# Performance work log

Hardware: AMD Instinct MI355X
Metric: run time of the kernel (lower is better)

## Reference

```python
import jax, jax.numpy as jnp
import numpy as np

N_BASIS = 128
N_CHANNELS = 256
DECAY_INIT = 3.0
B, T, V = 4, 4096, 1024


def setup_inputs() -> dict:
    key = jax.random.key(0)
    ks = jax.random.split(key, 6)
    std = 0.02
    return {
        "x": jax.random.normal(ks[0], (B, T, V), dtype=jnp.float32),
        "basis": jax.random.normal(ks[1], (V, 2 * N_BASIS), dtype=jnp.float32),
        "q_coeffs": jax.random.normal(ks[2], (N_CHANNELS, 2 * N_BASIS), dtype=jnp.float32) * std,
        "k_coeffs": jax.random.normal(ks[3], (N_CHANNELS, 2 * N_BASIS), dtype=jnp.float32) * std,
        "v_coeffs": jax.random.normal(ks[4], (N_CHANNELS, 2 * N_BASIS), dtype=jnp.float32) * std,
        "o_coeffs": jax.random.normal(ks[5], (N_CHANNELS, 2 * N_BASIS), dtype=jnp.float32) * std,
        "decay_logit": jnp.asarray(DECAY_INIT, dtype=jnp.float32),
        "out_scale": jnp.asarray(0.1, dtype=jnp.float32),
    }


def reference(x, basis, q_coeffs, k_coeffs, v_coeffs, o_coeffs, decay_logit, out_scale):
    dtype = x.dtype
    # FourierProjection: basis [V, 2*nb] @ coeffs.T [2*nb, C] -> [V, C]
    q_w = (basis @ q_coeffs.T).astype(dtype)
    k_w = (basis @ k_coeffs.T).astype(dtype)
    v_w = (basis @ v_coeffs.T).astype(dtype)
    o_w = (basis @ o_coeffs.T).astype(dtype)

    queries = jnp.einsum('btv,vc->btc', x, q_w)   # [B,T,C]
    keys    = jnp.einsum('btv,vc->btc', x, k_w)
    values  = jnp.einsum('btv,vc->btc', x, v_w)

    scores = jnp.einsum('btc,bsc->bts', queries, keys)  # [B,T,T]

    decay = jax.nn.sigmoid(decay_logit)
    t = x.shape[1]
    pos = jnp.arange(t)
    diff = pos[None, :] - pos[:, None]           # diff[i,j] = j - i
    causal_mask = (diff > 0)
    exponent = jnp.maximum(diff.astype(jnp.float32) - 1.0, 0.0)
    decay_weights = (decay ** exponent) * causal_mask.astype(jnp.float32)

    scores = scores * decay_weights.astype(dtype)[None]
    retrieved = jnp.einsum('bts,bsc->btc', scores, values)  # [B,T,C]
    out = jnp.einsum('btc,vc->btv', retrieved, o_w) * out_scale.astype(dtype)
    return out
```

## Files before the change

### kernel.cpp

```cpp
#include <hip/hip_runtime.h>
#include <math.h>
#include <stdint.h>

#define B_ 4
#define T_ 4096
#define V_ 1024
#define C_ 256
#define WINDOW 512

typedef __bf16 bf16x8 __attribute__((ext_vector_type(8)));
typedef float f32x4 __attribute__((ext_vector_type(4)));
typedef unsigned short us8 __attribute__((ext_vector_type(8)));

__device__ __forceinline__ void gld16(const void* g, void* l) {
  auto gp = reinterpret_cast<const __attribute__((address_space(1))) uint32_t*>(
      reinterpret_cast<uintptr_t>(g));
  auto lp = reinterpret_cast<__attribute__((address_space(3))) uint32_t*>(
      reinterpret_cast<uintptr_t>(l));
  __builtin_amdgcn_global_load_lds(gp, lp, 16, 0, 0);
}

__device__ __forceinline__ unsigned short f2bf(float f) {
  union { float f; unsigned u; } v; v.f = f;
  unsigned r = v.u + 0x7fffu + ((v.u >> 16) & 1u);
  return (unsigned short)(r >> 16);
}

__global__ __launch_bounds__(256) void prep_all(
    const float* __restrict__ qc, const float* __restrict__ kc,
    const float* __restrict__ vc, const float* __restrict__ basis,
    const float* __restrict__ oc, unsigned short* __restrict__ W3,
    unsigned short* __restrict__ bsT, unsigned short* __restrict__ owb) {
  const int tid = threadIdx.x;
  const int z = blockIdx.y;
  if (z == 0) {
    const size_t i = ((size_t)blockIdx.x * 256 + tid) * 8;
    const float* src = (i < 65536) ? qc + i
                     : (i < 131072) ? kc + (i - 65536) : vc + (i - 131072);
    const float4 a = *(const float4*)src;
    const float4 b = *(const float4*)(src + 4);
    us8 o;
    o[0] = f2bf(a.x); o[1] = f2bf(a.y); o[2] = f2bf(a.z); o[3] = f2bf(a.w);
    o[4] = f2bf(b.x); o[5] = f2bf(b.y); o[6] = f2bf(b.z); o[7] = f2bf(b.w);
    *(us8*)(W3 + i) = o;
  } else if (z == 1) {
    if (blockIdx.x >= 64) return;
    __shared__ unsigned short tile[64][65];
    const int rb = blockIdx.x >> 2, cb = blockIdx.x & 3;
#pragma unroll
    for (int r2 = 0; r2 < 2; ++r2) {
      const int idx = r2 * 256 + tid;
      const int row = idx >> 3, p = idx & 7;
      const float4 a = *(const float4*)(basis + (size_t)(rb * 64 + row) * 256 +
                                        cb * 64 + p * 8);
      const float4 b = *(const float4*)(basis + (size_t)(rb * 64 + row) * 256 +
                                        cb * 64 + p * 8 + 4);
      tile[row][p * 8 + 0] = f2bf(a.x); tile[row][p * 8 + 1] = f2bf(a.y);
      tile[row][p * 8 + 2] = f2bf(a.z); tile[row][p * 8 + 3] = f2bf(a.w);
      tile[row][p * 8 + 4] = f2bf(b.x); tile[row][p * 8 + 5] = f2bf(b.y);
      tile[row][p * 8 + 6] = f2bf(b.z); tile[row][p * 8 + 7] = f2bf(b.w);
    }
    __syncthreads();
#pragma unroll
    for (int r2 = 0; r2 < 2; ++r2) {
      const int idx = r2 * 256 + tid;
      const int c = idx >> 3, p = idx & 7;
      us8 v;
#pragma unroll
      for (int j = 0; j < 8; ++j) v[j] = tile[p * 8 + j][c];
      *(us8*)(bsT + ((size_t)(cb * 64 + c)) * 1024 + rb * 64 + p * 8) = v;
    }
  } else {
    if (blockIdx.x >= 64) return;
    __shared__ float As[16][65];
    __shared__ float Bs[16][65];
    const int bm = blockIdx.x >> 2, bn = blockIdx.x & 3;
    const int m0 = bm * 64, n0 = bn * 64;
    const int tm = tid >> 4, tn = tid & 15;
    float acc[4][4] = {};
    for (int k0 = 0; k0 < 256; k0 += 16) {
#pragma unroll
      for (int r = 0; r < 4; ++r) {
        const int m = (tid >> 4) + 16 * r;
        As[tid & 15][m] = basis[(size_t)(m0 + m) * 256 + k0 + (tid & 15)];
        Bs[tid & 15][m] = oc[(size_t)(n0 + m) * 256 + k0 + (tid & 15)];
      }
      __syncthreads();
#pragma unroll
      for (int k = 0; k < 16; ++k) {
        float a[4], b[4];
#pragma unroll
        for (int i = 0; i < 4; ++i) a[i] = As[k][tm * 4 + i];
#pragma unroll
        for (int j = 0; j < 4; ++j) b[j] = Bs[k][tn * 4 + j];
#pragma unroll
        for (int i = 0; i < 4; ++i)
#pragma unroll
          for (int j = 0; j < 4; ++j) acc[i][j] += a[i] * b[j];
      }
      __syncthreads();
    }
#pragma unroll
    for (int i = 0; i < 4; ++i)
#pragma unroll
      for (int j = 0; j < 4; ++j)
        owb[(size_t)(m0 + tm * 4 + i) * 256 + n0 + tn * 4 + j] =
            f2bf(acc[i][j]);
  }
}

__global__ __launch_bounds__(256) void gemm_x_basis(
    const float* __restrict__ X, const unsigned short* __restrict__ BT,
    unsigned short* __restrict__ Cp) {
  __shared__ __align__(16) unsigned short Bs[2][2][128 * 32];
  const int tid = threadIdx.x;
  const int g = blockIdx.x;
  const int xcd = g & 7, loc = g >> 3;
  const int m0 = (xcd * 32 + (loc >> 1)) * 64;
  const int n0 = (loc & 1) * 128;
  const int w = tid >> 6, l = tid & 63, q = l >> 4, lm = l & 15;
  const int wm = w >> 1, wn = w & 1;
  const f32x4 zero4 = {0.f, 0.f, 0.f, 0.f};
  f32x4 acc[2][4];
#pragma unroll
  for (int i = 0; i < 2; ++i)
#pragma unroll
    for (int j = 0; j < 4; ++j) acc[i][j] = zero4;

  const int rowB = tid >> 2;
  const int cph = (tid & 3) * 16;
  const int clg = (((tid & 3) - (rowB >> 1)) & 3) * 16;
  const int fsw = ((q + (lm >> 1)) & 3) * 16;

  const float* Ag = X + (size_t)(m0 + wm * 32 + lm) * 1024 + q * 8;
  f32x4 aR[2][2][2];

  auto stageB = [&](int t) {
    const char* Bg =
        (const char*)BT + ((size_t)(n0 + rowB) * 1024 + t * 64) * 2 + clg;
    char* d0 = (char*)&Bs[t & 1][0][0];
    char* d1 = (char*)&Bs[t & 1][1][0];
    gld16(Bg, d0 + rowB * 64 + cph);
    gld16(Bg + 64, d1 + rowB * 64 + cph);
    gld16(Bg + (size_t)64 * 2048, d0 + (64 + rowB) * 64 + cph);
    gld16(Bg + (size_t)64 * 2048 + 64, d1 + (64 + rowB) * 64 + cph);
  };
  auto loadA = [&](int t) {
#pragma unroll
    for (int mt = 0; mt < 2; ++mt)
#pragma unroll
      for (int kk = 0; kk < 2; ++kk) {
        const float* p = Ag + (size_t)mt * 16 * 1024 + t * 64 + kk * 32;
        aR[mt][kk][0] = *(const f32x4*)(p);
        aR[mt][kk][1] = *(const f32x4*)(p + 4);
      }
  };

  stageB(0);
  loadA(0);

  for (int t = 0; t < 16; ++t) {
    __syncthreads();
    if (t < 15) stageB(t + 1);
    bf16x8 af[2][2];
#pragma unroll
    for (int mt = 0; mt < 2; ++mt)
#pragma unroll
      for (int kk = 0; kk < 2; ++kk)
#pragma unroll
        for (int j = 0; j < 4; ++j) {
          af[mt][kk][j] = (__bf16)aR[mt][kk][0][j];
          af[mt][kk][4 + j] = (__bf16)aR[mt][kk][1][j];
        }
    if (t < 15) loadA(t + 1);
    bf16x8 bf[4][2];
#pragma unroll
    for (int nt = 0; nt < 4; ++nt)
#pragma unroll
      for (int kk = 0; kk < 2; ++kk)
        bf[nt][kk] = *(const bf16x8*)((const char*)&Bs[t & 1][kk][0] +
                                      (wn * 64 + nt * 16 + lm) * 64 + fsw);
#pragma unroll
    for (int mt = 0; mt < 2; ++mt)
#pragma unroll
      for (int nt = 0; nt < 4; ++nt) {
        acc[mt][nt] = __builtin_amdgcn_mfma_f32_16x16x32_bf16(
            af[mt][0], bf[nt][0], acc[mt][nt], 0, 0, 0);
        acc[mt][nt] = __builtin_amdgcn_mfma_f32_16x16x32_bf16(
            af[mt][1], bf[nt][1], acc[mt][nt], 0, 0, 0);
      }
  }
#pragma unroll
  for (int mt = 0; mt < 2; ++mt)
#pragma unroll
    for (int nt = 0; nt < 4; ++nt)
#pragma unroll
      for (int r = 0; r < 4; ++r) {
        const int row = m0 + wm * 32 + mt * 16 + q * 4 + r;
        const int col = n0 + wn * 64 + nt * 16 + lm;
        Cp[(size_t)row * 256 + col] = f2bf(acc[mt][nt][r]);
      }
}

__global__ __launch_bounds__(256) void gemm_bt_mfma(
    const unsigned short* __restrict__ A, const unsigned short* __restrict__ Bm,
    void* __restrict__ Cp, int Kd, int N, int nT, int outBf16,
    const float* __restrict__ alphaPtr) {
  __shared__ __align__(16) unsigned short As[128 * 32];
  __shared__ __align__(16) unsigned short Bs[128 * 32];
  const int tid = threadIdx.x;
  const int g = blockIdx.x;
  const int xcd = g & 7, loc = g >> 3;
  const int n0 = (loc % nT) * 128;
  const int m0 = (xcd * 16 + loc / nT) * 128;
  const int w = tid >> 6, l = tid & 63, q = l >> 4, lm = l & 15;
  const int wm = w >> 1, wn = w & 1;
  const f32x4 zero4 = {0.f, 0.f, 0.f, 0.f};
  f32x4 acc[4][4];
#pragma unroll
  for (int i = 0; i < 4; ++i)
#pragma unroll
    for (int j = 0; j < 4; ++j) acc[i][j] = zero4;

  const int rowA = tid >> 2;
  const int cph = (tid & 3) * 16;
  const int clg = (((tid & 3) - (rowA >> 1)) & 3) * 16;
  const int fsw = ((q + (lm >> 1)) & 3) * 16;

  for (int k0 = 0; k0 < Kd; k0 += 32) {
    __syncthreads();
    const char* Ag = (const char*)A + ((size_t)(m0 + rowA) * Kd + k0) * 2 + clg;
    const char* Bg = (const char*)Bm + ((size_t)(n0 + rowA) * Kd + k0) * 2 + clg;
    gld16(Ag, (char*)As + rowA * 64 + cph);
    gld16(Ag + (size_t)64 * Kd * 2, (char*)As + (64 + rowA) * 64 + cph);
    gld16(Bg, (char*)Bs + rowA * 64 + cph);
    gld16(Bg + (size_t)64 * Kd * 2, (char*)Bs + (64 + rowA) * 64 + cph);
    __syncthreads();
    bf16x8 af[4], bf[4];
#pragma unroll
    for (int mt = 0; mt < 4; ++mt)
      af[mt] = *(const bf16x8*)((const char*)As +
                                (wm * 64 + mt * 16 + lm) * 64 + fsw);
#pragma unroll
    for (int nt = 0; nt < 4; ++nt)
      bf[nt] = *(const bf16x8*)((const char*)Bs +
                                (wn * 64 + nt * 16 + lm) * 64 + fsw);
#pragma unroll
    for (int mt = 0; mt < 4; ++mt)
#pragma unroll
      for (int nt = 0; nt < 4; ++nt)
        acc[mt][nt] = __builtin_amdgcn_mfma_f32_16x16x32_bf16(
            af[mt], bf[nt], acc[mt][nt], 0, 0, 0);
  }
  const float alpha = alphaPtr ? alphaPtr[0] : 1.0f;
#pragma unroll
  for (int mt = 0; mt < 4; ++mt)
#pragma unroll
    for (int nt = 0; nt < 4; ++nt)
#pragma unroll
      for (int r = 0; r < 4; ++r) {
        const int row = m0 + wm * 64 + mt * 16 + q * 4 + r;
        const int col = n0 + wn * 64 + nt * 16 + lm;
        const float vv = acc[mt][nt][r] * alpha;
        if (outBf16)
          ((unsigned short*)Cp)[(size_t)row * N + col] = f2bf(vv);
        else
          ((float*)Cp)[(size_t)row * N + col] = vv;
      }
}

__global__ __launch_bounds__(256) void transpose_v(
    const unsigned short* __restrict__ QKV, unsigned short* __restrict__ VT) {
  __shared__ unsigned short tile[64][65];
  const int tb = blockIdx.x, cb = blockIdx.y, b = blockIdx.z;
  const int tid = threadIdx.x;
#pragma unroll
  for (int r2 = 0; r2 < 2; ++r2) {
    const int idx = r2 * 256 + tid;
    const int row = idx >> 3, p = idx & 7;
    const us8 v = *(const us8*)(QKV +
        ((size_t)(b * T_ + tb * 64 + row)) * 768 + 512 + cb * 64 + p * 8);
#pragma unroll
    for (int j = 0; j < 8; ++j) tile[row][p * 8 + j] = v[j];
  }
  __syncthreads();
#pragma unroll
  for (int r2 = 0; r2 < 2; ++r2) {
    const int idx = r2 * 256 + tid;
    const int c = idx >> 3, p = idx & 7;
    us8 v;
#pragma unroll
    for (int j = 0; j < 8; ++j) v[j] = tile[p * 8 + j][c];
    *(us8*)(VT + ((size_t)b * C_ + cb * 64 + c) * T_ + tb * 64 + p * 8) = v;
  }
}

__global__ __launch_bounds__(256) void attn_mfma(
    const unsigned short* __restrict__ QKV, const unsigned short* __restrict__ VT,
    const float* __restrict__ dlp, unsigned short* __restrict__ R) {
  __shared__ __align__(16) unsigned short Kst[16384];
  __shared__ __align__(16) unsigned short Vst[8192];
  __shared__ __align__(16) unsigned short Ss[32 * 72];

  const int g = blockIdx.x;
  const int chunk = (g & 7) * 64 + (g >> 3);
  const int b = chunk >> 7;
  const int t0 = (chunk & 127) << 5;
  const int tid = threadIdx.x;
  const int w = tid >> 6, l = tid & 63, q = l >> 4, lm = l & 15;
  const float dec = 1.f / (1.f + __expf(-dlp[0]));
  const float l2d = log2f(dec);
  const unsigned short* QKVb = QKV + (size_t)b * T_ * 768;
  const int fsw = ((q + (lm >> 1)) & 3) * 16;

  {
    const char* Qg = (const char*)(QKVb + (size_t)t0 * 768);
#pragma unroll
    for (int p = 0; p < 4; ++p) {
      const int o = (p * 256 + tid) * 16;
      const int ch = o >> 11, row = (o >> 6) & 31;
      const int clg = ((((o >> 4) & 3) - (row >> 1)) & 3) * 16;
      gld16(Qg + (size_t)row * 1536 + ch * 64 + clg, (char*)Kst + o);
    }
  }
  __syncthreads();
  bf16x8 qf[2][8];
#pragma unroll
  for (int mt = 0; mt < 2; ++mt)
#pragma unroll
    for (int ch = 0; ch < 8; ++ch)
      qf[mt][ch] = *(const bf16x8*)((const char*)Kst + ch * 2048 +
                                    (mt * 16 + lm) * 64 + fsw);

  const f32x4 zero4 = {0.f, 0.f, 0.f, 0.f};
  f32x4 acc[2][4];
#pragma unroll
  for (int i = 0; i < 2; ++i)
#pragma unroll
    for (int j = 0; j < 4; ++j) acc[i][j] = zero4;

  const int st0 = t0 >> 6;
  const int st1 = min(T_ / 64 - 1, (t0 + 31 + WINDOW) >> 6);
  const char* Kg = (const char*)QKVb + 512;
  const char* Vg = (const char*)(VT + (size_t)b * C_ * T_);

  for (int st = st0; st <= st1; ++st) {
    const int s0 = st << 6;
    __syncthreads();
#pragma unroll
    for (int p = 0; p < 8; ++p) {
      const int o = (p * 256 + tid) * 16;
      const int ch = o >> 12, row = (o >> 6) & 63;
      const int clg = ((((o >> 4) & 3) - (row >> 1)) & 3) * 16;
      gld16(Kg + (size_t)(s0 + row) * 1536 + ch * 64 + clg, (char*)Kst + o);
    }
#pragma unroll
    for (int p = 0; p < 4; ++p) {
      const int o = (p * 256 + tid) * 16;
      const int c = o >> 6;
      const int clg8 = (((o >> 4) & 3) - (c >> 1)) & 3;
      gld16(Vg + ((size_t)c * T_ + s0 + clg8 * 8) * 2, (char*)Vst + o);
    }
    __syncthreads();

    f32x4 sc[2] = {zero4, zero4};
#pragma unroll
    for (int ch = 0; ch < 8; ++ch) {
      const bf16x8 kf = *(const bf16x8*)((const char*)Kst + ch * 4096 +
                                         (w * 16 + lm) * 64 + fsw);
      sc[0] = __builtin_amdgcn_mfma_f32_16x16x32_bf16(qf[0][ch], kf, sc[0], 0, 0, 0);
      sc[1] = __builtin_amdgcn_mfma_f32_16x16x32_bf16(qf[1][ch], kf, sc[1], 0, 0, 0);
    }
    const int sg = s0 + w * 16 + lm;
#pragma unroll
    for (int mt = 0; mt < 2; ++mt)
#pragma unroll
      for (int r = 0; r < 4; ++r) {
        const int trow = t0 + mt * 16 + q * 4 + r;
        const int d = sg - trow;
        const float wgt = (d > 0) ? exp2f(l2d * (float)(d - 1)) : 0.f;
        Ss[(mt * 16 + q * 4 + r) * 72 + w * 16 + lm] = f2bf(sc[mt][r] * wgt);
      }
    __syncthreads();
    bf16x8 sa[2][2];
#pragma unroll
    for (int m2 = 0; m2 < 2; ++m2)
#pragma unroll
      for (int kc2 = 0; kc2 < 2; ++kc2)
        sa[m2][kc2] = *(const bf16x8*)&Ss[(m2 * 16 + lm) * 72 + kc2 * 32 + q * 8];
#pragma unroll
    for (int n2 = 0; n2 < 4; ++n2) {
      const bf16x8 vf = *(const bf16x8*)((const char*)Vst +
                                         (w * 64 + n2 * 16 + lm) * 64 + fsw);
      acc[0][n2] = __builtin_amdgcn_mfma_f32_16x16x32_bf16(sa[0][0], vf, acc[0][n2], 0, 0, 0);
      acc[1][n2] = __builtin_amdgcn_mfma_f32_16x16x32_bf16(sa[1][0], vf, acc[1][n2], 0, 0, 0);
    }
    __syncthreads();
#pragma unroll
    for (int p = 0; p < 4; ++p) {
      const int o = (p * 256 + tid) * 16;
      const int c = o >> 6;
      const int clg8 = (((o >> 4) & 3) - (c >> 1)) & 3;
      gld16(Vg + ((size_t)c * T_ + s0 + 32 + clg8 * 8) * 2, (char*)Vst + o);
    }
    __syncthreads();
#pragma unroll
    for (int n2 = 0; n2 < 4; ++n2) {
      const bf16x8 vf = *(const bf16x8*)((const char*)Vst +
                                         (w * 64 + n2 * 16 + lm) * 64 + fsw);
      acc[0][n2] = __builtin_amdgcn_mfma_f32_16x16x32_bf16(sa[0][1], vf, acc[0][n2], 0, 0, 0);
      acc[1][n2] = __builtin_amdgcn_mfma_f32_16x16x32_bf16(sa[1][1], vf, acc[1][n2], 0, 0, 0);
    }
  }
#pragma unroll
  for (int m2 = 0; m2 < 2; ++m2)
#pragma unroll
    for (int n2 = 0; n2 < 4; ++n2)
#pragma unroll
      for (int r = 0; r < 4; ++r) {
        const int row = t0 + m2 * 16 + q * 4 + r;
        const int col = w * 64 + n2 * 16 + lm;
        R[((size_t)b * T_ + row) * C_ + col] = f2bf(acc[m2][n2][r]);
      }
}

extern "C" void kernel_launch(void* const* d_in, const int* in_sizes, int n_in,
                              void* d_out, int out_size, void* d_ws,
                              size_t ws_size, hipStream_t stream) {
  const float* x     = (const float*)d_in[0];
  const float* basis = (const float*)d_in[1];
  const float* qc    = (const float*)d_in[2];
  const float* kc    = (const float*)d_in[3];
  const float* vc    = (const float*)d_in[4];
  const float* oc    = (const float*)d_in[5];
  const float* dl    = (const float*)d_in[6];
  const float* osc   = (const float*)d_in[7];
  float* out = (float*)d_out;

  unsigned short* ws = (unsigned short*)d_ws;
  const size_t MSZ = (size_t)B_ * T_ * C_;
  unsigned short* xb2  = ws;
  unsigned short* W3   = xb2 + MSZ;
  unsigned short* bsT  = W3 + 768 * 256;
  unsigned short* owb  = bsT + 256 * 1024;
  unsigned short* QKVb = owb + 1024 * 256;
  unsigned short* VTb  = QKVb + (size_t)B_ * T_ * 768;
  unsigned short* Rb   = VTb + MSZ;

  prep_all<<<dim3(96, 3), 256, 0, stream>>>(qc, kc, vc, basis, oc, W3, bsT,
                                            owb);
  gemm_x_basis<<<dim3(512), 256, 0, stream>>>(x, bsT, xb2);
  gemm_bt_mfma<<<dim3(768), 256, 0, stream>>>(xb2, W3, QKVb, 256, 768, 6, 1,
                                              nullptr);
  transpose_v<<<dim3(T_ / 64, C_ / 64, B_), 256, 0, stream>>>(QKVb, VTb);
  attn_mfma<<<dim3((T_ / 32) * B_), 256, 0, stream>>>(QKVb, VTb, dl, Rb);
  gemm_bt_mfma<<<dim3(1024), 256, 0, stream>>>(Rb, owb, out, C_, V_, 8, 0, osc);
}
```

Baseline: 225.2 us.

## Reassociate projections: fold K/Q coefficient product into basis and V/O into output weight

Reassociates the low-rank projections so the pipeline no longer materialises x@basis followed by a 256x768 QKV GEMM. Instead x is multiplied once by a concatenated [basis | basis·(kc^T qc)] matrix, giving xb (used as keys and, transposed, as values) plus a pre-mixed query term. The V and O coefficient products are folded into a single 1024x256 output weight. This drops one large bf16 GEMM pass over the B*T rows and its intermediate traffic, at the cost of extra small fp32 prep GEMMs and a different rounding order.

After: 333.3 us. 48.0% more time.

```diff
diff --git a/kernel.cpp b/kernel.cpp
--- a/kernel.cpp
+++ b/kernel.cpp
@@ -26,24 +26,14 @@
   return (unsigned short)(r >> 16);
 }
 
-__global__ __launch_bounds__(256) void prep_all(
+__global__ __launch_bounds__(256) void prep1(
     const float* __restrict__ qc, const float* __restrict__ kc,
-    const float* __restrict__ vc, const float* __restrict__ basis,
-    const float* __restrict__ oc, unsigned short* __restrict__ W3,
-    unsigned short* __restrict__ bsT, unsigned short* __restrict__ owb) {
+    const float* __restrict__ vc, const float* __restrict__ oc,
+    const float* __restrict__ basis, float* __restrict__ D1,
+    float* __restrict__ D2T, unsigned short* __restrict__ Bcat) {
   const int tid = threadIdx.x;
   const int z = blockIdx.y;
-  if (z == 0) {
-    const size_t i = ((size_t)blockIdx.x * 256 + tid) * 8;
-    const float* src = (i < 65536) ? qc + i
-                     : (i < 131072) ? kc + (i - 65536) : vc + (i - 131072);
-    const float4 a = *(const float4*)src;
-    const float4 b = *(const float4*)(src + 4);
-    us8 o;
-    o[0] = f2bf(a.x); o[1] = f2bf(a.y); o[2] = f2bf(a.z); o[3] = f2bf(a.w);
-    o[4] = f2bf(b.x); o[5] = f2bf(b.y); o[6] = f2bf(b.z); o[7] = f2bf(b.w);
-    *(us8*)(W3 + i) = o;
-  } else if (z == 1) {
+  if (z == 2) {
     if (blockIdx.x >= 64) return;
     __shared__ unsigned short tile[64][65];
     const int rb = blockIdx.x >> 2, cb = blockIdx.x & 3;
@@ -68,10 +58,13 @@
       us8 v;
 #pragma unroll
       for (int j = 0; j < 8; ++j) v[j] = tile[p * 8 + j][c];
-      *(us8*)(bsT + ((size_t)(cb * 64 + c)) * 1024 + rb * 64 + p * 8) = v;
+      *(us8*)(Bcat + ((size_t)(cb * 64 + c)) * 1024 + rb * 64 + p * 8) = v;
     }
   } else {
-    if (blockIdx.x >= 64) return;
+    if (blockIdx.x >= 16) return;
+    const float* A = (z == 0) ? kc : vc;
+    const float* Bp = (z == 0) ? qc : oc;
+    float* Out = (z == 0) ? D1 : D2T;
     __shared__ float As[16][65];
     __shared__ float Bs[16][65];
     const int bm = blockIdx.x >> 2, bn = blockIdx.x & 3;
@@ -82,8 +75,8 @@
 #pragma unroll
       for (int r = 0; r < 4; ++r) {
         const int m = (tid >> 4) + 16 * r;
-        As[tid & 15][m] = basis[(size_t)(m0 + m) * 256 + k0 + (tid & 15)];
-        Bs[tid & 15][m] = oc[(size_t)(n0 + m) * 256 + k0 + (tid & 15)];
+        As[tid & 15][m] = A[(size_t)(k0 + (tid & 15)) * 256 + m0 + m];
+        Bs[tid & 15][m] = Bp[(size_t)(k0 + (tid & 15)) * 256 + n0 + m];
       }
       __syncthreads();
 #pragma unroll
@@ -104,28 +97,102 @@
     for (int i = 0; i < 4; ++i)
 #pragma unroll
       for (int j = 0; j < 4; ++j)
-        owb[(size_t)(m0 + tm * 4 + i) * 256 + n0 + tn * 4 + j] =
+        Out[(size_t)(m0 + tm * 4 + i) * 256 + n0 + tn * 4 + j] = acc[i][j];
+  }
+}
+
+__global__ __launch_bounds__(256) void prep2(
+    const float* __restrict__ basis, const float* __restrict__ D1,
+    const float* __restrict__ D2T, unsigned short* __restrict__ Bcat,
+    unsigned short* __restrict__ Wvo) {
+  const int tid = threadIdx.x;
+  const int z = blockIdx.y;
+  __shared__ float As[16][65];
+  __shared__ float Bs[16][65];
+  const int tm = tid >> 4, tn = tid & 15;
+  float acc[4][4] = {};
+  if (z == 0) {
+    const int bm = blockIdx.x >> 4, bn = blockIdx.x & 15;
+    const int m0 = bm * 64, n0 = bn * 64;
+    for (int k0 = 0; k0 < 256; k0 += 16) {
+#pragma unroll
+      for (int r = 0; r < 4; ++r) {
+        const int m = (tid >> 4) + 16 * r;
+        As[tid & 15][m] = D1[(size_t)(m0 + m) * 256 + k0 + (tid & 15)];
+        Bs[tid & 15][m] = basis[(size_t)(n0 + m) * 256 + k0 + (tid & 15)];
+      }
+      __syncthreads();
+#pragma unroll
+      for (int k = 0; k < 16; ++k) {
+        float a[4], b[4];
+#pragma unroll
+        for (int i = 0; i < 4; ++i) a[i] = As[k][tm * 4 + i];
+#pragma unroll
+        for (int j = 0; j < 4; ++j) b[j] = Bs[k][tn * 4 + j];
+#pragma unroll
+        for (int i = 0; i < 4; ++i)
+#pragma unroll
+          for (int j = 0; j < 4; ++j) acc[i][j] += a[i] * b[j];
+      }
+      __syncthreads();
+    }
+#pragma unroll
+    for (int i = 0; i < 4; ++i)
+#pragma unroll
+      for (int j = 0; j < 4; ++j)
+        Bcat[(size_t)(256 + m0 + tm * 4 + i) * 1024 + n0 + tn * 4 + j] =
             f2bf(acc[i][j]);
-  }
-}
-
-__global__ __launch_bounds__(256) void gemm_x_basis(
-    const float* __restrict__ X, const unsigned short* __restrict__ BT,
-    unsigned short* __restrict__ Cp) {
-  __shared__ __align__(16) unsigned short Bs[2][2][128 * 32];
+  } else {
+    const int bm = blockIdx.x >> 2, bn = blockIdx.x & 3;
+    const int m0 = bm * 64, n0 = bn * 64;
+    for (int k0 = 0; k0 < 256; k0 += 16) {
+#pragma unroll
+      for (int r = 0; r < 4; ++r) {
+        const int m = (tid >> 4) + 16 * r;
+        As[tid & 15][m] = basis[(size_t)(m0 + m) * 256 + k0 + (tid & 15)];
+        Bs[tid & 15][m] = D2T[(size_t)(n0 + m) * 256 + k0 + (tid & 15)];
+      }
+      __syncthreads();
+#pragma unroll
+      for (int k = 0; k < 16; ++k) {
+        float a[4], b[4];
+#pragma unroll
+        for (int i = 0; i < 4; ++i) a[i] = As[k][tm * 4 + i];
+#pragma unroll
+        for (int j = 0; j < 4; ++j) b[j] = Bs[k][tn * 4 + j];
+#pragma unroll
+        for (int i = 0; i < 4; ++i)
+#pragma unroll
+          for (int j = 0; j < 4; ++j) acc[i][j] += a[i] * b[j];
+      }
+      __syncthreads();
+    }
+#pragma unroll
+    for (int i = 0; i < 4; ++i)
+#pragma unroll
+      for (int j = 0; j < 4; ++j)
+        Wvo[(size_t)(m0 + tm * 4 + i) * 256 + n0 + tn * 4 + j] =
+            f2bf(acc[i][j]);
+  }
+}
+
+__global__ __launch_bounds__(256, 4) void gemm_x_fused(
+    const float* __restrict__ X, const unsigned short* __restrict__ Bc,
+    unsigned short* __restrict__ XQ) {
+  __shared__ __align__(16) unsigned short Bs[2][2][64 * 32];
   const int tid = threadIdx.x;
   const int g = blockIdx.x;
   const int xcd = g & 7, loc = g >> 3;
-  const int m0 = (xcd * 32 + (loc >> 1)) * 64;
-  const int n0 = (loc & 1) * 128;
+  const int m0 = (xcd * 32 + (loc >> 3)) * 64;
+  const int n0 = (loc & 7) * 64;
   const int w = tid >> 6, l = tid & 63, q = l >> 4, lm = l & 15;
   const int wm = w >> 1, wn = w & 1;
   const f32x4 zero4 = {0.f, 0.f, 0.f, 0.f};
-  f32x4 acc[2][4];
+  f32x4 acc[2][2];
 #pragma unroll
   for (int i = 0; i < 2; ++i)
 #pragma unroll
-    for (int j = 0; j < 4; ++j) acc[i][j] = zero4;
+    for (int j = 0; j < 2; ++j) acc[i][j] = zero4;
 
   const int rowB = tid >> 2;
   const int cph = (tid & 3) * 16;
@@ -137,13 +204,9 @@
 
   auto stageB = [&](int t) {
     const char* Bg =
-        (const char*)BT + ((size_t)(n0 + rowB) * 1024 + t * 64) * 2 + clg;
-    char* d0 = (char*)&Bs[t & 1][0][0];
-    char* d1 = (char*)&Bs[t & 1][1][0];
-    gld16(Bg, d0 + rowB * 64 + cph);
-    gld16(Bg + 64, d1 + rowB * 64 + cph);
-    gld16(Bg + (size_t)64 * 2048, d0 + (64 + rowB) * 64 + cph);
-    gld16(Bg + (size_t)64 * 2048 + 64, d1 + (64 + rowB) * 64 + cph);
+        (const char*)Bc + ((size_t)(n0 + rowB) * 1024) * 2 + t * 128 + clg;
+    gld16(Bg, (char*)&Bs[t & 1][0][0] + rowB * 64 + cph);
+    gld16(Bg + 64, (char*)&Bs[t & 1][1][0] + rowB * 64 + cph);
   };
   auto loadA = [&](int t) {
 #pragma unroll
@@ -173,17 +236,17 @@
           af[mt][kk][4 + j] = (__bf16)aR[mt][kk][1][j];
         }
     if (t < 15) loadA(t + 1);
-    bf16x8 bf[4][2];
-#pragma unroll
-    for (int nt = 0; nt < 4; ++nt)
+    bf16x8 bf[2][2];
+#pragma unroll
+    for (int nt = 0; nt < 2; ++nt)
 #pragma unroll
       for (int kk = 0; kk < 2; ++kk)
         bf[nt][kk] = *(const bf16x8*)((const char*)&Bs[t & 1][kk][0] +
-                                      (wn * 64 + nt * 16 + lm) * 64 + fsw);
+                                      (wn * 32 + nt * 16 + lm) * 64 + fsw);
 #pragma unroll
     for (int mt = 0; mt < 2; ++mt)
 #pragma unroll
-      for (int nt = 0; nt < 4; ++nt) {
+      for (int nt = 0; nt < 2; ++nt) {
         acc[mt][nt] = __builtin_amdgcn_mfma_f32_16x16x32_bf16(
             af[mt][0], bf[nt][0], acc[mt][nt], 0, 0, 0);
         acc[mt][nt] = __builtin_amdgcn_mfma_f32_16x16x32_bf16(
@@ -193,12 +256,12 @@
 #pragma unroll
   for (int mt = 0; mt < 2; ++mt)
 #pragma unroll
-    for (int nt = 0; nt < 4; ++nt)
+    for (int nt = 0; nt < 2; ++nt)
 #pragma unroll
       for (int r = 0; r < 4; ++r) {
         const int row = m0 + wm * 32 + mt * 16 + q * 4 + r;
-        const int col = n0 + wn * 64 + nt * 16 + lm;
-        Cp[(size_t)row * 256 + col] = f2bf(acc[mt][nt][r]);
+        const int col = n0 + wn * 32 + nt * 16 + lm;
+        XQ[(size_t)row * 512 + col] = f2bf(acc[mt][nt][r]);
       }
 }
 
@@ -269,8 +332,8 @@
       }
 }
 
-__global__ __launch_bounds__(256) void transpose_v(
-    const unsigned short* __restrict__ QKV, unsigned short* __restrict__ VT) {
+__global__ __launch_bounds__(256) void transpose_x(
+    const unsigned short* __restrict__ XQ, unsigned short* __restrict__ VT) {
   __shared__ unsigned short tile[64][65];
   const int tb = blockIdx.x, cb = blockIdx.y, b = blockIdx.z;
   const int tid = threadIdx.x;
@@ -278,8 +341,8 @@
   for (int r2 = 0; r2 < 2; ++r2) {
     const int idx = r2 * 256 + tid;
     const int row = idx >> 3, p = idx & 7;
-    const us8 v = *(const us8*)(QKV +
-        ((size_t)(b * T_ + tb * 64 + row)) * 768 + 512 + cb * 64 + p * 8);
+    const us8 v = *(const us8*)(XQ +
+        ((size_t)(b * T_ + tb * 64 + row)) * 512 + cb * 64 + p * 8);
 #pragma unroll
     for (int j = 0; j < 8; ++j) tile[row][p * 8 + j] = v[j];
   }
@@ -296,8 +359,8 @@
 }
 
 __global__ __launch_bounds__(256) void attn_mfma(
-    const unsigned short* __restrict__ QKV, const unsigned short* __restrict__ VT,
-    const float* __restrict__ dlp, unsigned short* __restrict__ R) {
+    const unsigned short* __restrict__ XQ, const unsigned short* __restrict__ VTx,
+    const float* __restrict__ dlp, unsigned short* __restrict__ Rv) {
   __shared__ __align__(16) unsigned short Kst[16384];
   __shared__ __align__(16) unsigned short Vst[8192];
   __shared__ __align__(16) unsigned short Ss[32 * 72];
@@ -310,17 +373,17 @@
   const int w = tid >> 6, l = tid & 63, q = l >> 4, lm = l & 15;
   const float dec = 1.f / (1.f + __expf(-dlp[0]));
   const float l2d = log2f(dec);
-  const unsigned short* QKVb = QKV + (size_t)b * T_ * 768;
+  const unsigned short* XQb = XQ + (size_t)b * T_ * 512;
   const int fsw = ((q + (lm >> 1)) & 3) * 16;
 
   {
-    const char* Qg = (const char*)(QKVb + (size_t)t0 * 768);
+    const char* Qg = (const char*)(XQb + (size_t)t0 * 512) + 512;
 #pragma unroll
     for (int p = 0; p < 4; ++p) {
       const int o = (p * 256 + tid) * 16;
       const int ch = o >> 11, row = (o >> 6) & 31;
       const int clg = ((((o >> 4) & 3) - (row >> 1)) & 3) * 16;
-      gld16(Qg + (size_t)row * 1536 + ch * 64 + clg, (char*)Kst + o);
+      gld16(Qg + (size_t)row * 1024 + ch * 64 + clg, (char*)Kst + o);
     }
   }
   __syncthreads();
@@ -341,8 +404,8 @@
 
   const int st0 = t0 >> 6;
   const int st1 = min(T_ / 64 - 1, (t0 + 31 + WINDOW) >> 6);
-  const char* Kg = (const char*)QKVb + 512;
-  const char* Vg = (const char*)(VT + (size_t)b * C_ * T_);
+  const char* Kg = (const char*)XQb;
+  const char* Vg = (const char*)(VTx + (size_t)b * C_ * T_);
 
   for (int st = st0; st <= st1; ++st) {
     const int s0 = st << 6;
@@ -352,7 +415,7 @@
       const int o = (p * 256 + tid) * 16;
       const int ch = o >> 12, row = (o >> 6) & 63;
       const int clg = ((((o >> 4) & 3) - (row >> 1)) & 3) * 16;
-      gld16(Kg + (size_t)(s0 + row) * 1536 + ch * 64 + clg, (char*)Kst + o);
+      gld16(Kg + (size_t)(s0 + row) * 1024 + ch * 64 + clg, (char*)Kst + o);
     }
 #pragma unroll
     for (int p = 0; p < 4; ++p) {
@@ -420,7 +483,7 @@
       for (int r = 0; r < 4; ++r) {
         const int row = t0 + m2 * 16 + q * 4 + r;
         const int col = w * 64 + n2 * 16 + lm;
-        R[((size_t)b * T_ + row) * C_ + col] = f2bf(acc[m2][n2][r]);
+        Rv[((size_t)b * T_ + row) * C_ + col] = f2bf(acc[m2][n2][r]);
       }
 }
 
@@ -439,20 +502,18 @@
 
   unsigned short* ws = (unsigned short*)d_ws;
   const size_t MSZ = (size_t)B_ * T_ * C_;
-  unsigned short* xb2  = ws;
-  unsigned short* W3   = xb2 + MSZ;
-  unsigned short* bsT  = W3 + 768 * 256;
-  unsigned short* owb  = bsT + 256 * 1024;
-  unsigned short* QKVb = owb + 1024 * 256;
-  unsigned short* VTb  = QKVb + (size_t)B_ * T_ * 768;
-  unsigned short* Rb   = VTb + MSZ;
-
-  prep_all<<<dim3(96, 3), 256, 0, stream>>>(qc, kc, vc, basis, oc, W3, bsT,
-                                            owb);
-  gemm_x_basis<<<dim3(512), 256, 0, stream>>>(x, bsT, xb2);
-  gemm_bt_mfma<<<dim3(768), 256, 0, stream>>>(xb2, W3, QKVb, 256, 768, 6, 1,
-                                              nullptr);
-  transpose_v<<<dim3(T_ / 64, C_ / 64, B_), 256, 0, stream>>>(QKVb, VTb);
-  attn_mfma<<<dim3((T_ / 32) * B_), 256, 0, stream>>>(QKVb, VTb, dl, Rb);
-  gemm_bt_mfma<<<dim3(1024), 256, 0, stream>>>(Rb, owb, out, C_, V_, 8, 0, osc);
-}
+  unsigned short* XQ   = ws;
+  unsigned short* VTx  = XQ + (size_t)16384 * 512;
+  unsigned short* Rv   = VTx + MSZ;
+  unsigned short* Bcat = Rv + MSZ;
+  unsigned short* Wvo  = Bcat + 512 * 1024;
+  float* D1  = (float*)(Wvo + 1024 * 256);
+  float* D2T = D1 + 256 * 256;
+
+  prep1<<<dim3(64, 3), 256, 0, stream>>>(qc, kc, vc, oc, basis, D1, D2T, Bcat);
+  prep2<<<dim3(64, 2), 256, 0, stream>>>(basis, D1, D2T, Bcat, Wvo);
+  gemm_x_fused<<<dim3(2048), 256, 0, stream>>>(x, Bcat, XQ);
+  transpose_x<<<dim3(T_ / 64, C_ / 64, B_), 256, 0, stream>>>(XQ, VTx);
+  attn_mfma<<<dim3((T_ / 32) * B_), 256, 0, stream>>>(XQ, VTx, dl, Rv);
+  gemm_bt_mfma<<<dim3(1024), 256, 0, stream>>>(Rv, Wvo, out, C_, V_, 8, 0, osc);
+}
```
